# Optimization experiments

Measured on AMD Instinct MI355X. Metric: run time of the kernel, lower is better.

Reference implementation:

```python
import jax, jax.numpy as jnp
import numpy as np

N, E, F, NC, G = 50000, 400000, 128, 10, 64
EPS_BN = 1e-5
NEG_SLOPE = 0.2


def gat_conv(x, src, dst, W, a_src, a_dst, b, H, C):
    # PyG GATConv (concat=True): h = xW reshaped [N,H,C]; edge score =
    # leaky_relu(a_src.h_j + a_dst.h_i); softmax over incoming edges of i;
    # out_i = sum_j alpha_ij * h_j, then bias.
    n = x.shape[0]
    h = (x @ W).reshape(n, H, C)
    s_src = jnp.sum(h * a_src, axis=-1)  # [N,H]
    s_dst = jnp.sum(h * a_dst, axis=-1)  # [N,H]
    e = jax.nn.leaky_relu(s_src[src] + s_dst[dst], NEG_SLOPE)  # [E',H]
    m = jax.ops.segment_max(e, dst, num_segments=n)
    e = jnp.exp(e - m[dst])
    z = jax.ops.segment_sum(e, dst, num_segments=n)
    alpha = e / (z[dst] + 1e-16)
    msg = h[src] * alpha[:, :, None]  # [E',H,C]
    out = jax.ops.segment_sum(msg, dst, num_segments=n)
    return out.reshape(n, H * C) + b


def batch_norm(x, g, b):
    mu = jnp.mean(x, axis=0)
    var = jnp.var(x, axis=0)
    return g * (x - mu) * jax.lax.rsqrt(var + EPS_BN) + b


def setup_inputs() -> dict:
    key = jax.random.key(0)
    ks = jax.random.split(key, 32)
    d = {}
    d["x"] = jax.random.normal(ks[0], (N, F), dtype=jnp.float32)
    d["edge_index"] = jax.random.randint(ks[1], (2, E), 0, N, dtype=jnp.int32)
    d["batch"] = jnp.sort(jax.random.randint(ks[2], (N,), 0, G, dtype=jnp.int32))

    def nrm(k, shape, scale=0.1):
        return jax.random.normal(k, shape, dtype=jnp.float32) * scale

    # GATConv1: F -> 16, heads=20
    d["W1"] = nrm(ks[3], (F, 20 * 16))
    d["as1"] = nrm(ks[4], (20, 16))
    d["ad1"] = nrm(ks[5], (20, 16))
    d["b1"] = jnp.zeros((320,), jnp.float32)
    d["g1"], d["be1"] = jnp.ones((320,), jnp.float32), jnp.zeros((320,), jnp.float32)
    d["lw1"], d["lb1"] = nrm(ks[6], (320, 16)), jnp.zeros((16,), jnp.float32)
    d["gl1"], d["bel1"] = jnp.ones((16,), jnp.float32), jnp.zeros((16,), jnp.float32)
    # GATConv2: 16 -> 32, heads=16
    d["W2"] = nrm(ks[7], (16, 16 * 32))
    d["as2"] = nrm(ks[8], (16, 32))
    d["ad2"] = nrm(ks[9], (16, 32))
    d["b2"] = jnp.zeros((512,), jnp.float32)
    d["g2"], d["be2"] = jnp.ones((512,), jnp.float32), jnp.zeros((512,), jnp.float32)
    d["lw2"], d["lb2"] = nrm(ks[10], (512, 32)), jnp.zeros((32,), jnp.float32)
    d["gl2"], d["bel2"] = jnp.ones((32,), jnp.float32), jnp.zeros((32,), jnp.float32)
    # GATConv3: 32 -> 48, heads=8
    d["W3"] = nrm(ks[11], (32, 8 * 48))
    d["as3"] = nrm(ks[12], (8, 48))
    d["ad3"] = nrm(ks[13], (8, 48))
    d["b3"] = jnp.zeros((384,), jnp.float32)
    d["g3"], d["be3"] = jnp.ones((384,), jnp.float32), jnp.zeros((384,), jnp.float32)
    d["lwf"], d["lbf"] = nrm(ks[14], (384, NC)), jnp.zeros((NC,), jnp.float32)
    return d


def reference(x, edge_index, batch, W1, as1, ad1, b1, g1, be1, lw1, lb1, gl1, bel1,
              W2, as2, ad2, b2, g2, be2, lw2, lb2, gl2, bel2,
              W3, as3, ad3, b3, g3, be3, lwf, lbf):
    n = x.shape[0]
    loops = jnp.arange(n, dtype=edge_index.dtype)
    src = jnp.concatenate([edge_index[0], loops])
    dst = jnp.concatenate([edge_index[1], loops])

    h = gat_conv(x, src, dst, W1, as1, ad1, b1, 20, 16)
    h = jax.nn.relu(batch_norm(h, g1, be1))
    h = h @ lw1 + lb1
    h = jax.nn.relu(batch_norm(h, gl1, bel1))

    h = gat_conv(h, src, dst, W2, as2, ad2, b2, 16, 32)
    h = jax.nn.relu(batch_norm(h, g2, be2))
    h = h @ lw2 + lb2
    h = jax.nn.relu(batch_norm(h, gl2, bel2))

    h = gat_conv(h, src, dst, W3, as3, ad3, b3, 8, 48)
    h = jax.nn.relu(batch_norm(h, g3, be3))

    # global_mean_pool over graph ids
    sums = jax.ops.segment_sum(h, batch, num_segments=G)
    cnts = jax.ops.segment_sum(jnp.ones((n,), h.dtype), batch, num_segments=G)
    pooled = sums / jnp.maximum(cnts, 1.0)[:, None]
    # dropout is identity in eval mode
    return pooled @ lwf + lbf
```

## Files before the change

kernel.cpp:

```cpp
#include <hip/hip_runtime.h>
#include <cstdint>
#include <cstddef>

#define N_NODES 50000
#define N_EDGES 400000
#define TOT_E   450000
#define G_GRAPHS 64
#define PB 2048
#define SCAN_B 98

typedef unsigned short u16;
typedef unsigned int u32;
typedef unsigned char u8;
typedef __attribute__((ext_vector_type(8))) short s16x8;
typedef __attribute__((ext_vector_type(4))) float f32x4;
typedef __attribute__((ext_vector_type(2))) float f32x2;

__device__ __forceinline__ float b2f(u16 v) {
    union { u32 u; float f; } x; x.u = ((u32)v) << 16; return x.f;
}
__device__ __forceinline__ float lo2f(u32 u) {
    union { u32 u; float f; } x; x.u = u << 16; return x.f;
}
__device__ __forceinline__ float hi2f(u32 u) {
    union { u32 u; float f; } x; x.u = u & 0xffff0000u; return x.f;
}
__device__ __forceinline__ u16 f2b(float f) {
    union { float f; u32 u; } x; x.f = f;
    u32 r = x.u + 0x7fffu + ((x.u >> 16) & 1u);
    return (u16)(r >> 16);
}
__device__ __forceinline__ u32 pack2(float a, float b) {
    return (u32)f2b(a) | ((u32)f2b(b) << 16);
}

__global__ void k_init_deg(int* __restrict__ deg) {
    int i = blockIdx.x * blockDim.x + threadIdx.x;
    if (i < N_NODES) deg[i] = 1;
}

__global__ void k_hist(const int* __restrict__ ei, int* __restrict__ deg) {
    int e = blockIdx.x * blockDim.x + threadIdx.x;
    if (e < N_EDGES) atomicAdd(&deg[ei[N_EDGES + e]], 1);
}

__global__ void k_scan1(const int* __restrict__ deg, int* __restrict__ rowptr,
                        int* __restrict__ bsum) {
    __shared__ int buf[512];
    int tid = threadIdx.x;
    int i = blockIdx.x * 512 + tid;
    int v = (i < N_NODES) ? deg[i] : 0;
    buf[tid] = v;
    __syncthreads();
    for (int off = 1; off < 512; off <<= 1) {
        int t = (tid >= off) ? buf[tid - off] : 0;
        __syncthreads();
        buf[tid] += t;
        __syncthreads();
    }
    if (i < N_NODES) rowptr[i] = buf[tid] - v;
    if (tid == 511) bsum[blockIdx.x] = buf[511];
}

__global__ void k_scan2(int* __restrict__ bsum) {
    __shared__ int buf[128];
    int tid = threadIdx.x;
    int v = (tid < SCAN_B) ? bsum[tid] : 0;
    buf[tid] = v;
    __syncthreads();
    for (int off = 1; off < 128; off <<= 1) {
        int t = (tid >= off) ? buf[tid - off] : 0;
        __syncthreads();
        buf[tid] += t;
        __syncthreads();
    }
    if (tid < SCAN_B) bsum[tid] = buf[tid] - v;
}

__global__ void k_scan3(int* __restrict__ rowptr, int* __restrict__ cursor,
                        const int* __restrict__ bsum) {
    int i = blockIdx.x * blockDim.x + threadIdx.x;
    if (i < N_NODES) {
        int v = rowptr[i] + bsum[i >> 9];
        rowptr[i] = v;
        cursor[i] = v;
    }
    if (i == 0) rowptr[N_NODES] = TOT_E;
}

__global__ void k_scatter(const int* __restrict__ ei, int* __restrict__ cursor,
                          int* __restrict__ col, int* __restrict__ cdst) {
    int e = blockIdx.x * blockDim.x + threadIdx.x;
    if (e < N_EDGES) {
        int s = ei[e], d = ei[N_EDGES + e];
        int p = atomicAdd(&cursor[d], 1);
        col[p] = s;
        cdst[p] = d;
    } else if (e < TOT_E) {
        int i = e - N_EDGES;
        int p = atomicAdd(&cursor[i], 1);
        col[p] = i;
        cdst[p] = i;
    }
}

template<int K, int NO>
__global__ void k_wpack(const float* __restrict__ W, u16* __restrict__ Bp) {
    constexpr int KC = (K + 31) / 32;
    constexpr int NT = NO / 16;
    int idx = blockIdx.x * 256 + threadIdx.x;
    if (idx >= KC * NT * 64) return;
    int lane = idx & 63;
    int t = (idx >> 6) % NT;
    int c = (idx >> 6) / NT;
    int n = t * 16 + (lane & 15);
    int kbase = c * 32 + (lane >> 4) * 8;
    u16 v[8];
#pragma unroll
    for (int j = 0; j < 8; j++) {
        int k = kbase + j;
        v[j] = (k < K) ? f2b(W[(size_t)k * NO + n]) : (u16)0;
    }
    *(uint4*)(Bp + (size_t)idx * 8) = *(const uint4*)v;
}

template<int K, int NO, int H, int C>
__global__ void k_wtilde(const float* __restrict__ W, const float* __restrict__ as,
                         const float* __restrict__ ad, float* __restrict__ wts,
                         float* __restrict__ wtd) {
    int t = threadIdx.x;
    if (t >= K * H) return;
    int k = t / H, h = t - k * H;
    float s1 = 0.f, s2 = 0.f;
    for (int c = 0; c < C; c++) {
        float wv = W[(size_t)k * NO + h * C + c];
        s1 = fmaf(wv, as[h * C + c], s1);
        s2 = fmaf(wv, ad[h * C + c], s2);
    }
    wts[h * K + k] = s1;
    wtd[h * K + k] = s2;
}

template<int K>
__global__ void k_xform(const u16* __restrict__ X, const float* __restrict__ sc,
                        const float* __restrict__ sh, u16* __restrict__ Xt) {
    constexpr int NO2 = K / 2;
    int t = blockIdx.x * blockDim.x + threadIdx.x;
    if (t >= N_NODES * NO2) return;
    int w = t % NO2;
    u32 u = ((const u32*)X)[t];
    float2 scv = *(const float2*)&sc[2 * w];
    float2 shv = *(const float2*)&sh[2 * w];
    float a = fmaxf(lo2f(u) * scv.x + shv.x, 0.f);
    float b = fmaxf(hi2f(u) * scv.y + shv.y, 0.f);
    ((u32*)Xt)[t] = pack2(a, b);
}

template<int K, int H>
__global__ void k_scores_x(const u16* __restrict__ Xt, const float* __restrict__ wts,
                           const float* __restrict__ wtd, float* __restrict__ ssrc,
                           float* __restrict__ sdst) {
    int t = blockIdx.x * blockDim.x + threadIdx.x;
    if (t >= N_NODES * H) return;
    int i = t / H, h = t - i * H;
    const uint4* r = (const uint4*)(Xt + (size_t)i * K);
    const float4* ws = (const float4*)(wts + h * K);
    const float4* wd = (const float4*)(wtd + h * K);
    float s1 = 0.f, s2 = 0.f;
#pragma unroll
    for (int c8 = 0; c8 < K / 8; c8++) {
        uint4 u = r[c8];
        float v0 = lo2f(u.x), v1 = hi2f(u.x), v2 = lo2f(u.y), v3 = hi2f(u.y);
        float v4 = lo2f(u.z), v5 = hi2f(u.z), v6 = lo2f(u.w), v7 = hi2f(u.w);
        float4 aa = ws[c8 * 2], ab = ws[c8 * 2 + 1];
        float4 da = wd[c8 * 2], db = wd[c8 * 2 + 1];
        s1 = fmaf(v0, aa.x, fmaf(v1, aa.y, fmaf(v2, aa.z, fmaf(v3, aa.w, s1))));
        s1 = fmaf(v4, ab.x, fmaf(v5, ab.y, fmaf(v6, ab.z, fmaf(v7, ab.w, s1))));
        s2 = fmaf(v0, da.x, fmaf(v1, da.y, fmaf(v2, da.z, fmaf(v3, da.w, s2))));
        s2 = fmaf(v4, db.x, fmaf(v5, db.y, fmaf(v6, db.z, fmaf(v7, db.w, s2))));
    }
    ssrc[t] = s1;
    sdst[t] = s2;
}

template<int H, int K>
__global__ void k_aggx(const u16* __restrict__ Xt, const float* __restrict__ ssrc,
                       const float* __restrict__ sdst, const int* __restrict__ rowptr,
                       const int* __restrict__ col, u16* __restrict__ M) {
    constexpr int WPR = K / 2;
    constexpr int EPR = 64 / WPR;
    constexpr int Q = K / 4;
    static_assert(H * K == 256, "m row must be 256 elems (4/lane)");
    int wid = (int)((blockIdx.x * blockDim.x + threadIdx.x) >> 6);
    int lane = threadIdx.x & 63;
    if (wid >= N_NODES) return;
    int hl = lane / Q;
    int q = lane % Q;
    int lslot = lane / WPR;
    int lword = lane % WPR;
    float sd = (lane < H) ? sdst[(size_t)wid * H + lane] : 0.f;
    float a0 = 0.f, a1 = 0.f, a2 = 0.f, a3 = 0.f;
    float z = 0.f;
    int beg = rowptr[wid], end = rowptr[wid + 1];
    for (int base = beg; base < end; base += 64) {
        int nmax = min(64, end - base);
        int myc = (base + lane < end) ? col[base + lane] : 0;
        int j = 0;
        for (; j + EPR <= nmax; j += EPR) {
            int ce = __shfl(myc, j + lslot);
            u32 g = *(const u32*)(Xt + (size_t)ce * K + lword * 2);
            int se[EPR];
#pragma unroll
            for (int e = 0; e < EPR; e++) se[e] = __shfl(myc, j + e);
            float w[EPR];
#pragma unroll
            for (int e = 0; e < EPR; e++) w[e] = 0.f;
            if (lane < H) {
#pragma unroll
                for (int e = 0; e < EPR; e++) {
                    float v = ssrc[(size_t)se[e] * H + lane] + sd;
                    v = (v > 0.f) ? v : 0.2f * v;
                    w[e] = __expf(v);
                    z += w[e];
                }
            }
#pragma unroll
            for (int e = 0; e < EPR; e++) {
                float al = __shfl(w[e], hl);
                u32 xa = __shfl(g, e * WPR + 2 * q);
                u32 xb = __shfl(g, e * WPR + 2 * q + 1);
                a0 = fmaf(al, lo2f(xa), a0);
                a1 = fmaf(al, hi2f(xa), a1);
                a2 = fmaf(al, lo2f(xb), a2);
                a3 = fmaf(al, hi2f(xb), a3);
            }
        }
        for (; j < nmax; j++) {
            int se = __shfl(myc, j);
            u32 g = *(const u32*)(Xt + (size_t)se * K + lword * 2);
            float w0 = 0.f;
            if (lane < H) {
                float v = ssrc[(size_t)se * H + lane] + sd;
                v = (v > 0.f) ? v : 0.2f * v;
                w0 = __expf(v);
                z += w0;
            }
            float al = __shfl(w0, hl);
            u32 xa = __shfl(g, 2 * q);
            u32 xb = __shfl(g, 2 * q + 1);
            a0 = fmaf(al, lo2f(xa), a0);
            a1 = fmaf(al, hi2f(xa), a1);
            a2 = fmaf(al, lo2f(xb), a2);
            a3 = fmaf(al, hi2f(xb), a3);
        }
    }
    float zk = __shfl(z, hl);
    float inv = 1.0f / (zk + 1e-16f);
    uint2 o;
    o.x = pack2(a0 * inv, a1 * inv);
    o.y = pack2(a2 * inv, a3 * inv);
    u32* orow = (u32*)(M + (size_t)wid * (H * K));
    *(uint2*)&orow[hl * WPR + 2 * q] = o;
}

template<int K, int NO, int C>
__global__ __launch_bounds__(256, 2)
void k_gemmd(const u16* __restrict__ M, const u16* __restrict__ Bp,
             const float* __restrict__ wb, u16* __restrict__ Y) {
    constexpr int NT = NO / 16;
    constexpr int HK = (NO / C) * K;
    int lane = threadIdx.x & 63;
    int wv = __builtin_amdgcn_readfirstlane((int)(threadIdx.x >> 6));
    int rbase = blockIdx.x * 64 + wv * 16;
    int m = lane & 15, quad = lane >> 4;
    int arow = rbase + m;
    if (arow >= N_NODES) arow = N_NODES - 1;
    const u16* xr = M + (size_t)arow * HK;
#pragma unroll
    for (int t = 0; t < NT; t++) {
        int h = (t * 16) / C;
        s16x8 a;
        if (K == 32 || quad < 2) {
            a = *(const s16x8*)(xr + h * K + quad * 8);
        } else {
#pragma unroll
            for (int j = 0; j < 8; j++) a[j] = 0;
        }
        s16x8 b = *(const s16x8*)(Bp + ((size_t)(t * 64 + lane)) * 8);
        f32x4 acc = (f32x4){0.f, 0.f, 0.f, 0.f};
        acc = __builtin_amdgcn_mfma_f32_16x16x32_bf16(a, b, acc, 0, 0, 0);
        int colb = t * 16 + m;
        float bv = wb[colb];
#pragma unroll
        for (int i = 0; i < 4; i++) {
            int grow = rbase + quad * 4 + i;
            if (grow < N_NODES) Y[(size_t)grow * NO + colb] = f2b(acc[i] + bv);
        }
    }
}

template<int K, int NO, bool XFORM>
__global__ __launch_bounds__(256, 2)
void k_gemm(const float* __restrict__ X, const u16* __restrict__ Bp,
            const float* __restrict__ scale, const float* __restrict__ shift,
            u16* __restrict__ Y) {
    constexpr int KC = (K + 31) / 32;
    constexpr int NT = NO / 16;
    int lane = threadIdx.x & 63;
    int wv = __builtin_amdgcn_readfirstlane((int)(threadIdx.x >> 6));
    int rbase = blockIdx.x * 64 + wv * 16;
    int m = lane & 15, quad = lane >> 4;
    int arow = rbase + m;
    if (arow >= N_NODES) arow = N_NODES - 1;
    const float* xr = X + (size_t)arow * K;

    f32x4 acc[NT];
#pragma unroll
    for (int t = 0; t < NT; t++) acc[t] = (f32x4){0.f, 0.f, 0.f, 0.f};

    for (int c = 0; c < KC; c++) {
        int kbase = c * 32 + quad * 8;
        float xv[8];
        if (kbase < K) {
            float4 va = *(const float4*)&xr[kbase];
            float4 vb = *(const float4*)&xr[kbase + 4];
            xv[0] = va.x; xv[1] = va.y; xv[2] = va.z; xv[3] = va.w;
            xv[4] = vb.x; xv[5] = vb.y; xv[6] = vb.z; xv[7] = vb.w;
            if (XFORM) {
                float4 sa = *(const float4*)&scale[kbase];
                float4 sb = *(const float4*)&scale[kbase + 4];
                float4 ha = *(const float4*)&shift[kbase];
                float4 hb = *(const float4*)&shift[kbase + 4];
                xv[0] = fmaxf(xv[0] * sa.x + ha.x, 0.f);
                xv[1] = fmaxf(xv[1] * sa.y + ha.y, 0.f);
                xv[2] = fmaxf(xv[2] * sa.z + ha.z, 0.f);
                xv[3] = fmaxf(xv[3] * sa.w + ha.w, 0.f);
                xv[4] = fmaxf(xv[4] * sb.x + hb.x, 0.f);
                xv[5] = fmaxf(xv[5] * sb.y + hb.y, 0.f);
                xv[6] = fmaxf(xv[6] * sb.z + hb.z, 0.f);
                xv[7] = fmaxf(xv[7] * sb.w + hb.w, 0.f);
            }
        } else {
#pragma unroll
            for (int j = 0; j < 8; j++) xv[j] = 0.f;
        }
        s16x8 a;
#pragma unroll
        for (int j = 0; j < 8; j++) a[j] = (short)f2b(xv[j]);

        const u16* bp = Bp + (size_t)(c * NT) * 64 * 8;
#pragma unroll
        for (int t = 0; t < NT; t++) {
            s16x8 b = *(const s16x8*)(bp + ((size_t)(t * 64 + lane)) * 8);
            acc[t] = __builtin_amdgcn_mfma_f32_16x16x32_bf16(a, b, acc[t], 0, 0, 0);
        }
    }

#pragma unroll
    for (int t = 0; t < NT; t++) {
        int colb = t * 16 + m;
#pragma unroll
        for (int i = 0; i < 4; i++) {
            int grow = rbase + quad * 4 + i;
            if (grow < N_NODES) Y[(size_t)grow * NO + colb] = f2b(acc[t][i]);
        }
    }
}

template<int K, int NO, bool XFORM, bool BIAS>
__global__ __launch_bounds__(256, 2)
void k_gemmb(const u16* __restrict__ X, const u16* __restrict__ Bp,
             const float* __restrict__ scale, const float* __restrict__ shift,
             const float* __restrict__ wb, u16* __restrict__ Y) {
    constexpr int KC = (K + 31) / 32;
    constexpr int NT = NO / 16;
    int lane = threadIdx.x & 63;
    int wv = __builtin_amdgcn_readfirstlane((int)(threadIdx.x >> 6));
    int rbase = blockIdx.x * 64 + wv * 16;
    int m = lane & 15, quad = lane >> 4;
    int arow = rbase + m;
    if (arow >= N_NODES) arow = N_NODES - 1;
    const u32* xr = (const u32*)(X + (size_t)arow * K);

    f32x4 acc[NT];
#pragma unroll
    for (int t = 0; t < NT; t++) acc[t] = (f32x4){0.f, 0.f, 0.f, 0.f};

    for (int c = 0; c < KC; c++) {
        int kbase = c * 32 + quad * 8;
        s16x8 a;
        if (kbase < K) {
            uint4 w = *(const uint4*)&xr[kbase >> 1];
            if (XFORM) {
                float xv[8];
                xv[0] = lo2f(w.x); xv[1] = hi2f(w.x);
                xv[2] = lo2f(w.y); xv[3] = hi2f(w.y);
                xv[4] = lo2f(w.z); xv[5] = hi2f(w.z);
                xv[6] = lo2f(w.w); xv[7] = hi2f(w.w);
                float4 sa = *(const float4*)&scale[kbase];
                float4 sb = *(const float4*)&scale[kbase + 4];
                float4 ha = *(const float4*)&shift[kbase];
                float4 hb = *(const float4*)&shift[kbase + 4];
                xv[0] = fmaxf(xv[0] * sa.x + ha.x, 0.f);
                xv[1] = fmaxf(xv[1] * sa.y + ha.y, 0.f);
                xv[2] = fmaxf(xv[2] * sa.z + ha.z, 0.f);
                xv[3] = fmaxf(xv[3] * sa.w + ha.w, 0.f);
                xv[4] = fmaxf(xv[4] * sb.x + hb.x, 0.f);
                xv[5] = fmaxf(xv[5] * sb.y + hb.y, 0.f);
                xv[6] = fmaxf(xv[6] * sb.z + hb.z, 0.f);
                xv[7] = fmaxf(xv[7] * sb.w + hb.w, 0.f);
#pragma unroll
                for (int j = 0; j < 8; j++) a[j] = (short)f2b(xv[j]);
            } else {
                a = *(const s16x8*)&w;
            }
        } else {
#pragma unroll
            for (int j = 0; j < 8; j++) a[j] = 0;
        }

        const u16* bp = Bp + (size_t)(c * NT) * 64 * 8;
#pragma unroll
        for (int t = 0; t < NT; t++) {
            s16x8 b = *(const s16x8*)(bp + ((size_t)(t * 64 + lane)) * 8);
            acc[t] = __builtin_amdgcn_mfma_f32_16x16x32_bf16(a, b, acc[t], 0, 0, 0);
        }
    }

#pragma unroll
    for (int t = 0; t < NT; t++) {
        int colb = t * 16 + m;
        float bv = BIAS ? wb[colb] : 0.f;
#pragma unroll
        for (int i = 0; i < 4; i++) {
            int grow = rbase + quad * 4 + i;
            if (grow < N_NODES) Y[(size_t)grow * NO + colb] = f2b(acc[t][i] + bv);
        }
    }
}

template<int H, int C>
__global__ void k_scores(const u16* __restrict__ Hm, const float* __restrict__ asrc,
                         const float* __restrict__ adst, float* __restrict__ ssrc,
                         float* __restrict__ sdst, u8* __restrict__ H8) {
    static_assert(C == 16, "fp8 emit assumes C==16");
    int t = blockIdx.x * blockDim.x + threadIdx.x;
    if (t >= N_NODES * H) return;
    int i = t / H, h = t - i * H;
    const uint4* row4 = (const uint4*)(Hm + (size_t)i * H * C + h * C);
    const float4* a4 = (const float4*)(asrc + h * C);
    const float4* d4 = (const float4*)(adst + h * C);
    float s1 = 0.f, s2 = 0.f;
    uint4 q8;
    u32* qw = (u32*)&q8;
#pragma unroll
    for (int c8 = 0; c8 < C / 8; c8++) {
        uint4 u = row4[c8];
        float v0 = lo2f(u.x), v1 = hi2f(u.x), v2 = lo2f(u.y), v3 = hi2f(u.y);
        float v4 = lo2f(u.z), v5 = hi2f(u.z), v6 = lo2f(u.w), v7 = hi2f(u.w);
        float4 aa = a4[c8 * 2], ab = a4[c8 * 2 + 1];
        float4 da = d4[c8 * 2], db = d4[c8 * 2 + 1];
        s1 = fmaf(v0, aa.x, fmaf(v1, aa.y, fmaf(v2, aa.z, fmaf(v3, aa.w, s1))));
        s1 = fmaf(v4, ab.x, fmaf(v5, ab.y, fmaf(v6, ab.z, fmaf(v7, ab.w, s1))));
        s2 = fmaf(v0, da.x, fmaf(v1, da.y, fmaf(v2, da.z, fmaf(v3, da.w, s2))));
        s2 = fmaf(v4, db.x, fmaf(v5, db.y, fmaf(v6, db.z, fmaf(v7, db.w, s2))));
        u32 qa = 0, qb = 0;
        qa = __builtin_amdgcn_cvt_pk_fp8_f32(v0, v1, qa, false);
        qa = __builtin_amdgcn_cvt_pk_fp8_f32(v2, v3, qa, true);
        qb = __builtin_amdgcn_cvt_pk_fp8_f32(v4, v5, qb, false);
        qb = __builtin_amdgcn_cvt_pk_fp8_f32(v6, v7, qb, true);
        qw[c8 * 2] = qa;
        qw[c8 * 2 + 1] = qb;
    }
    ssrc[t] = s1;
    sdst[t] = s2;
    *(uint4*)(H8 + (size_t)i * (H * C) + h * C) = q8;
}

template<int H, int C>
__global__ void k_agg8(const u8* __restrict__ Hm8, const float* __restrict__ ssrc,
                       const float* __restrict__ sdst, const int* __restrict__ rowptr,
                       const int* __restrict__ col, const float* __restrict__ bias,
                       u16* __restrict__ out) {
    constexpr int HC = H * C;
    constexpr int W2 = HC / 8;
    static_assert(W2 <= 64, "row must fit 64 uint2");
    static_assert((C % 8) == 0, "8-col block must stay within one head");
    int wid = (int)((blockIdx.x * blockDim.x + threadIdx.x) >> 6);
    int lane = threadIdx.x & 63;
    if (wid >= N_NODES) return;
    int hl = (8 * lane) / C;
    int gidx = (lane < W2) ? lane : 0;
    float sd = (lane < H) ? sdst[(size_t)wid * H + lane] : 0.f;
    float acc[8];
#pragma unroll
    for (int q = 0; q < 8; q++) acc[q] = 0.f;
    float z = 0.f;
    int beg = rowptr[wid], end = rowptr[wid + 1];
    for (int base = beg; base < end; base += 64) {
        int nmax = min(64, end - base);
        int myc = (base + lane < end) ? col[base + lane] : 0;
        int j = 0;
        for (; j + 4 <= nmax; j += 4) {
            int s0 = __shfl(myc, j), s1 = __shfl(myc, j + 1);
            int s2 = __shfl(myc, j + 2), s3 = __shfl(myc, j + 3);
            uint2 g0 = ((const uint2*)(Hm8 + (size_t)s0 * HC))[gidx];
            uint2 g1 = ((const uint2*)(Hm8 + (size_t)s1 * HC))[gidx];
            uint2 g2 = ((const uint2*)(Hm8 + (size_t)s2 * HC))[gidx];
            uint2 g3 = ((const uint2*)(Hm8 + (size_t)s3 * HC))[gidx];
            float w0 = 0.f, w1 = 0.f, w2 = 0.f, w3 = 0.f;
            if (lane < H) {
                float v0 = ssrc[(size_t)s0 * H + lane] + sd;
                float v1 = ssrc[(size_t)s1 * H + lane] + sd;
                float v2 = ssrc[(size_t)s2 * H + lane] + sd;
                float v3 = ssrc[(size_t)s3 * H + lane] + sd;
                v0 = (v0 > 0.f) ? v0 : 0.2f * v0;
                v1 = (v1 > 0.f) ? v1 : 0.2f * v1;
                v2 = (v2 > 0.f) ? v2 : 0.2f * v2;
                v3 = (v3 > 0.f) ? v3 : 0.2f * v3;
                w0 = __expf(v0); w1 = __expf(v1);
                w2 = __expf(v2); w3 = __expf(v3);
                z += (w0 + w1) + (w2 + w3);
            }
            float wk0 = __shfl(w0, hl), wk1 = __shfl(w1, hl);
            float wk2 = __shfl(w2, hl), wk3 = __shfl(w3, hl);
            f32x2 p;
            p = __builtin_amdgcn_cvt_pk_f32_fp8(g0.x, false);
            acc[0] = fmaf(wk0, p.x, acc[0]); acc[1] = fmaf(wk0, p.y, acc[1]);
            p = __builtin_amdgcn_cvt_pk_f32_fp8(g0.x, true);
            acc[2] = fmaf(wk0, p.x, acc[2]); acc[3] = fmaf(wk0, p.y, acc[3]);
            p = __builtin_amdgcn_cvt_pk_f32_fp8(g0.y, false);
            acc[4] = fmaf(wk0, p.x, acc[4]); acc[5] = fmaf(wk0, p.y, acc[5]);
            p = __builtin_amdgcn_cvt_pk_f32_fp8(g0.y, true);
            acc[6] = fmaf(wk0, p.x, acc[6]); acc[7] = fmaf(wk0, p.y, acc[7]);
            p = __builtin_amdgcn_cvt_pk_f32_fp8(g1.x, false);
            acc[0] = fmaf(wk1, p.x, acc[0]); acc[1] = fmaf(wk1, p.y, acc[1]);
            p = __builtin_amdgcn_cvt_pk_f32_fp8(g1.x, true);
            acc[2] = fmaf(wk1, p.x, acc[2]); acc[3] = fmaf(wk1, p.y, acc[3]);
            p = __builtin_amdgcn_cvt_pk_f32_fp8(g1.y, false);
            acc[4] = fmaf(wk1, p.x, acc[4]); acc[5] = fmaf(wk1, p.y, acc[5]);
            p = __builtin_amdgcn_cvt_pk_f32_fp8(g1.y, true);
            acc[6] = fmaf(wk1, p.x, acc[6]); acc[7] = fmaf(wk1, p.y, acc[7]);
            p = __builtin_amdgcn_cvt_pk_f32_fp8(g2.x, false);
            acc[0] = fmaf(wk2, p.x, acc[0]); acc[1] = fmaf(wk2, p.y, acc[1]);
            p = __builtin_amdgcn_cvt_pk_f32_fp8(g2.x, true);
            acc[2] = fmaf(wk2, p.x, acc[2]); acc[3] = fmaf(wk2, p.y, acc[3]);
            p = __builtin_amdgcn_cvt_pk_f32_fp8(g2.y, false);
            acc[4] = fmaf(wk2, p.x, acc[4]); acc[5] = fmaf(wk2, p.y, acc[5]);
            p = __builtin_amdgcn_cvt_pk_f32_fp8(g2.y, true);
            acc[6] = fmaf(wk2, p.x, acc[6]); acc[7] = fmaf(wk2, p.y, acc[7]);
            p = __builtin_amdgcn_cvt_pk_f32_fp8(g3.x, false);
            acc[0] = fmaf(wk3, p.x, acc[0]); acc[1] = fmaf(wk3, p.y, acc[1]);
            p = __builtin_amdgcn_cvt_pk_f32_fp8(g3.x, true);
            acc[2] = fmaf(wk3, p.x, acc[2]); acc[3] = fmaf(wk3, p.y, acc[3]);
            p = __builtin_amdgcn_cvt_pk_f32_fp8(g3.y, false);
            acc[4] = fmaf(wk3, p.x, acc[4]); acc[5] = fmaf(wk3, p.y, acc[5]);
            p = __builtin_amdgcn_cvt_pk_f32_fp8(g3.y, true);
            acc[6] = fmaf(wk3, p.x, acc[6]); acc[7] = fmaf(wk3, p.y, acc[7]);
        }
        for (; j < nmax; j++) {
            int s0 = __shfl(myc, j);
            uint2 g0 = ((const uint2*)(Hm8 + (size_t)s0 * HC))[gidx];
            float w0 = 0.f;
            if (lane < H) {
                float v = ssrc[(size_t)s0 * H + lane] + sd;
                v = (v > 0.f) ? v : 0.2f * v;
                w0 = __expf(v);
                z += w0;
            }
            float wk0 = __shfl(w0, hl);
            f32x2 p;
            p = __builtin_amdgcn_cvt_pk_f32_fp8(g0.x, false);
            acc[0] = fmaf(wk0, p.x, acc[0]); acc[1] = fmaf(wk0, p.y, acc[1]);
            p = __builtin_amdgcn_cvt_pk_f32_fp8(g0.x, true);
            acc[2] = fmaf(wk0, p.x, acc[2]); acc[3] = fmaf(wk0, p.y, acc[3]);
            p = __builtin_amdgcn_cvt_pk_f32_fp8(g0.y, false);
            acc[4] = fmaf(wk0, p.x, acc[4]); acc[5] = fmaf(wk0, p.y, acc[5]);
            p = __builtin_amdgcn_cvt_pk_f32_fp8(g0.y, true);
            acc[6] = fmaf(wk0, p.x, acc[6]); acc[7] = fmaf(wk0, p.y, acc[7]);
        }
    }
    float zk = __shfl(z, hl);
    if (lane < W2) {
        float inv = 1.0f / (zk + 1e-16f);
        const float4* b4 = (const float4*)(bias + 8 * lane);
        float4 ba = b4[0], bb = b4[1];
        uint4 o;
        o.x = pack2(fmaf(acc[0], inv, ba.x), fmaf(acc[1], inv, ba.y));
        o.y = pack2(fmaf(acc[2], inv, ba.z), fmaf(acc[3], inv, ba.w));
        o.z = pack2(fmaf(acc[4], inv, bb.x), fmaf(acc[5], inv, bb.y));
        o.w = pack2(fmaf(acc[6], inv, bb.z), fmaf(acc[7], inv, bb.w));
        ((uint4*)(out + (size_t)wid * HC))[lane] = o;
    }
}

template<int NO>
__global__ void k_bnstats(const u16* __restrict__ X, float* __restrict__ psum,
                          float* __restrict__ psumsq) {
    constexpr int NO2 = NO / 2;
    constexpr int RPS = (NO2 >= 256) ? 1 : ((255 + NO2) / NO2);
    constexpr int BS = NO2 * RPS;
    __shared__ float2 ls[BS], ls2[BS];
    int c2 = threadIdx.x % NO2;
    int rsub = threadIdx.x / NO2;
    constexpr int chunk = (N_NODES + PB - 1) / PB;
    int r0 = blockIdx.x * chunk;
    int r1 = min(N_NODES, r0 + chunk);
    float2 s = make_float2(0.f, 0.f), s2 = make_float2(0.f, 0.f);
    const u32* Xw = (const u32*)X;
#pragma unroll 4
    for (int r = r0 + rsub; r < r1; r += RPS) {
        u32 u = Xw[(size_t)r * NO2 + c2];
        float a = lo2f(u), b = hi2f(u);
        s.x += a; s.y += b;
        s2.x += a * a; s2.y += b * b;
    }
    if (RPS > 1) {
        ls[threadIdx.x] = s;
        ls2[threadIdx.x] = s2;
        __syncthreads();
        for (int off = BS / 2; off >= NO2; off >>= 1) {
            if (threadIdx.x < off) {
                ls[threadIdx.x].x += ls[threadIdx.x + off].x;
                ls[threadIdx.x].y += ls[threadIdx.x + off].y;
                ls2[threadIdx.x].x += ls2[threadIdx.x + off].x;
                ls2[threadIdx.x].y += ls2[threadIdx.x + off].y;
            }
            __syncthreads();
        }
        s = ls[threadIdx.x];
        s2 = ls2[threadIdx.x];
    }
    if (rsub == 0) {
        *(float2*)&psum[(size_t)blockIdx.x * NO + 2 * c2] = s;
        *(float2*)&psumsq[(size_t)blockIdx.x * NO + 2 * c2] = s2;
    }
}

__global__ void k_bnfinal(const float* __restrict__ psum, const float* __restrict__ psumsq,
                          const float* __restrict__ g, const float* __restrict__ be,
                          float* __restrict__ scale, float* __restrict__ shift, int NO) {
    __shared__ float s1[256], s2[256];
    int col = blockIdx.x;
    int tid = threadIdx.x;
    float a = 0.f, b = 0.f;
    for (int bk = tid; bk < PB; bk += 256) {
        a += psum[(size_t)bk * NO + col];
        b += psumsq[(size_t)bk * NO + col];
    }
    s1[tid] = a;
    s2[tid] = b;
    __syncthreads();
    for (int off = 128; off > 0; off >>= 1) {
        if (tid < off) {
            s1[tid] += s1[tid + off];
            s2[tid] += s2[tid + off];
        }
        __syncthreads();
    }
    if (tid == 0) {
        float mu = s1[0] / (float)N_NODES;
        float var = s2[0] / (float)N_NODES - mu * mu;
        float sc = g[col] * rsqrtf(var + 1e-5f);
        scale[col] = sc;
        shift[col] = be[col] - mu * sc;
    }
}

__global__ void k_bhist(const int* __restrict__ batch, int* __restrict__ cnt) {
    __shared__ int h[G_GRAPHS];
    int tid = threadIdx.x;
    if (tid < G_GRAPHS) h[tid] = 0;
    __syncthreads();
    int i = blockIdx.x * blockDim.x + tid;
    if (i < N_NODES) atomicAdd(&h[batch[i]], 1);
    __syncthreads();
    if (tid < G_GRAPHS) atomicAdd(&cnt[tid], h[tid]);
}

__global__ void k_pool(const u16* __restrict__ X, const int* __restrict__ batch,
                       const float* __restrict__ sc, const float* __restrict__ sh,
                       float* __restrict__ pooled) {
    int t2 = threadIdx.x;
    const int chunk = (N_NODES + gridDim.x - 1) / gridDim.x;
    int r0 = blockIdx.x * chunk;
    int r1 = min(N_NODES, r0 + chunk);
    if (r0 >= N_NODES) return;
    float2 scv = *(const float2*)&sc[2 * t2];
    float2 shv = *(const float2*)&sh[2 * t2];
    const u32* Xw = (const u32*)X;
    float2 acc = make_float2(0.f, 0.f);
    int cur = batch[r0];
    for (int r = r0; r < r1; r++) {
        int gid = batch[r];
        if (gid != cur) {
            atomicAdd(&pooled[(size_t)cur * 384 + 2 * t2], acc.x);
            atomicAdd(&pooled[(size_t)cur * 384 + 2 * t2 + 1], acc.y);
            acc = make_float2(0.f, 0.f);
            cur = gid;
        }
        u32 u = Xw[(size_t)r * 192 + t2];
        acc.x += fmaxf(lo2f(u) * scv.x + shv.x, 0.f);
        acc.y += fmaxf(hi2f(u) * scv.y + shv.y, 0.f);
    }
    atomicAdd(&pooled[(size_t)cur * 384 + 2 * t2], acc.x);
    atomicAdd(&pooled[(size_t)cur * 384 + 2 * t2 + 1], acc.y);
}

__global__ void k_final(const float* __restrict__ pooled, const int* __restrict__ cnt,
                        const float* __restrict__ lwf, const float* __restrict__ lbf,
                        float* __restrict__ out) {
    int t = threadIdx.x;
    if (t >= G_GRAPHS * 10) return;
    int g = t / 10, c = t - g * 10;
    float inv = 1.0f / fmaxf((float)cnt[g], 1.0f);
    float acc = lbf[c];
    for (int k = 0; k < 384; k++)
        acc = fmaf(pooled[(size_t)g * 384 + k] * inv, lwf[k * 10 + c], acc);
    out[t] = acc;
}

extern "C" void kernel_launch(void* const* d_in, const int* in_sizes, int n_in,
                              void* d_out, int out_size, void* d_ws, size_t ws_size,
                              hipStream_t stream) {
    const float* x    = (const float*)d_in[0];
    const int*   ei   = (const int*)d_in[1];
    const int*   batch= (const int*)d_in[2];
    const float* W1   = (const float*)d_in[3];
    const float* as1  = (const float*)d_in[4];
    const float* ad1  = (const float*)d_in[5];
    const float* b1   = (const float*)d_in[6];
    const float* g1   = (const float*)d_in[7];
    const float* be1  = (const float*)d_in[8];
    const float* lw1  = (const float*)d_in[9];
    const float* lb1  = (const float*)d_in[10];
    const float* gl1  = (const float*)d_in[11];
    const float* bel1 = (const float*)d_in[12];
    const float* W2   = (const float*)d_in[13];
    const float* as2  = (const float*)d_in[14];
    const float* ad2  = (const float*)d_in[15];
    const float* b2   = (const float*)d_in[16];
    const float* g2   = (const float*)d_in[17];
    const float* be2  = (const float*)d_in[18];
    const float* lw2  = (const float*)d_in[19];
    const float* lb2  = (const float*)d_in[20];
    const float* gl2  = (const float*)d_in[21];
    const float* bel2 = (const float*)d_in[22];
    const float* W3   = (const float*)d_in[23];
    const float* as3  = (const float*)d_in[24];
    const float* ad3  = (const float*)d_in[25];
    const float* b3   = (const float*)d_in[26];
    const float* g3   = (const float*)d_in[27];
    const float* be3  = (const float*)d_in[28];
    const float* lwf  = (const float*)d_in[29];
    const float* lbf  = (const float*)d_in[30];
    float* out = (float*)d_out;

    char* p = (char*)d_ws;
    auto alloc = [&](size_t bytes) {
        char* r = p;
        p += (bytes + 255) & ~(size_t)255;
        return r;
    };
    int*   rowptr = (int*)alloc(4 * (size_t)(N_NODES + 1));
    int*   cursor = (int*)alloc(4 * (size_t)N_NODES);
    int*   deg    = (int*)alloc(4 * (size_t)N_NODES);
    int*   bsum   = (int*)alloc(4 * (size_t)(SCAN_B + 1));
    int*   col    = (int*)alloc(4 * (size_t)TOT_E);
    int*   cdst   = (int*)alloc(4 * (size_t)TOT_E);
    float* ssrc   = (float*)alloc(4 * (size_t)N_NODES * 20);
    float* sdst   = (float*)alloc(4 * (size_t)N_NODES * 20);
    u16*   hbuf   = (u16*)alloc(2 * (size_t)N_NODES * 512);
    u16*   obuf   = (u16*)alloc(2 * (size_t)N_NODES * 512);
    u16*   xbuf   = (u16*)alloc(2 * (size_t)N_NODES * 32);
    u16*   xtil   = (u16*)alloc(2 * (size_t)N_NODES * 32);
    u8*    hbuf8  = (u8*)alloc((size_t)N_NODES * 320);
    float* psum   = (float*)alloc(4 * (size_t)PB * 512);
    float* psumsq = (float*)alloc(4 * (size_t)PB * 512);
    float* scA    = (float*)alloc(4 * 512);
    float* shA    = (float*)alloc(4 * 512);
    float* scB    = (float*)alloc(4 * 64);
    float* shB    = (float*)alloc(4 * 64);
    float* wts    = (float*)alloc(4 * 256);
    float* wtd    = (float*)alloc(4 * 256);
    float* pooled = (float*)alloc(4 * (size_t)G_GRAPHS * 384);
    int*   cnt    = (int*)alloc(4 * G_GRAPHS);
    u16*   bp1    = (u16*)alloc(2 * (size_t)4 * 20 * 64 * 8);
    u16*   bp2    = (u16*)alloc(2 * (size_t)1 * 32 * 64 * 8);
    u16*   bp3    = (u16*)alloc(2 * (size_t)1 * 24 * 64 * 8);
    u16*   bpl1   = (u16*)alloc(2 * (size_t)10 * 1 * 64 * 8);
    u16*   bpl2   = (u16*)alloc(2 * (size_t)16 * 2 * 64 * 8);
    u16*   mbuf   = hbuf;

    const int LB = (N_NODES + 63) / 64;

    k_init_deg<<<(N_NODES + 255) / 256, 256, 0, stream>>>(deg);
    k_hist<<<(N_EDGES + 255) / 256, 256, 0, stream>>>(ei, deg);
    k_scan1<<<SCAN_B, 512, 0, stream>>>(deg, rowptr, bsum);
    k_scan2<<<1, 128, 0, stream>>>(bsum);
    k_scan3<<<(N_NODES + 255) / 256, 256, 0, stream>>>(rowptr, cursor, bsum);
    k_scatter<<<(TOT_E + 255) / 256, 256, 0, stream>>>(ei, cursor, col, cdst);
    k_wpack<128, 320><<<20, 256, 0, stream>>>(W1, bp1);
    k_wpack<16, 512><<<8, 256, 0, stream>>>(W2, bp2);
    k_wpack<32, 384><<<6, 256, 0, stream>>>(W3, bp3);
    k_wpack<320, 16><<<3, 256, 0, stream>>>(lw1, bpl1);
    k_wpack<512, 32><<<8, 256, 0, stream>>>(lw2, bpl2);
    hipMemsetAsync(pooled, 0, 4 * (size_t)G_GRAPHS * 384 + 256, stream);

    k_gemm<128, 320, false><<<LB, 256, 0, stream>>>(x, bp1, nullptr, nullptr, hbuf);
    k_scores<20, 16><<<(N_NODES * 20 + 255) / 256, 256, 0, stream>>>(hbuf, as1, ad1, ssrc, sdst, hbuf8);
    k_agg8<20, 16><<<(N_NODES + 3) / 4, 256, 0, stream>>>(hbuf8, ssrc, sdst, rowptr, col, b1, obuf);
    k_bnstats<320><<<PB, 320, 0, stream>>>(obuf, psum, psumsq);
    k_bnfinal<<<320, 256, 0, stream>>>(psum, psumsq, g1, be1, scA, shA, 320);
    k_gemmb<320, 16, true, true><<<LB, 256, 0, stream>>>(obuf, bpl1, scA, shA, lb1, xbuf);
    k_bnstats<16><<<PB, 256, 0, stream>>>(xbuf, psum, psumsq);
    k_bnfinal<<<16, 256, 0, stream>>>(psum, psumsq, gl1, bel1, scB, shB, 16);

    k_wtilde<16, 512, 16, 32><<<1, 256, 0, stream>>>(W2, as2, ad2, wts, wtd);
    k_xform<16><<<(N_NODES * 8 + 255) / 256, 256, 0, stream>>>(xbuf, scB, shB, xtil);
    k_scores_x<16, 16><<<(N_NODES * 16 + 255) / 256, 256, 0, stream>>>(xtil, wts, wtd, ssrc, sdst);
    k_aggx<16, 16><<<(N_NODES + 3) / 4, 256, 0, stream>>>(xtil, ssrc, sdst, rowptr, col, mbuf);
    k_gemmd<16, 512, 32><<<LB, 256, 0, stream>>>(mbuf, bp2, b2, obuf);
    k_bnstats<512><<<PB, 256, 0, stream>>>(obuf, psum, psumsq);
    k_bnfinal<<<512, 256, 0, stream>>>(psum, psumsq, g2, be2, scA, shA, 512);
    k_gemmb<512, 32, true, true><<<LB, 256, 0, stream>>>(obuf, bpl2, scA, shA, lb2, xbuf);
    k_bnstats<32><<<PB, 256, 0, stream>>>(xbuf, psum, psumsq);
    k_bnfinal<<<32, 256, 0, stream>>>(psum, psumsq, gl2, bel2, scB, shB, 32);

    k_wtilde<32, 384, 8, 48><<<1, 256, 0, stream>>>(W3, as3, ad3, wts, wtd);
    k_xform<32><<<(N_NODES * 16 + 255) / 256, 256, 0, stream>>>(xbuf, scB, shB, xtil);
    k_scores_x<32, 8><<<(N_NODES * 8 + 255) / 256, 256, 0, stream>>>(xtil, wts, wtd, ssrc, sdst);
    k_aggx<8, 32><<<(N_NODES + 3) / 4, 256, 0, stream>>>(xtil, ssrc, sdst, rowptr, col, mbuf);
    k_gemmd<32, 384, 48><<<LB, 256, 0, stream>>>(mbuf, bp3, b3, obuf);
    k_bnstats<384><<<PB, 384, 0, stream>>>(obuf, psum, psumsq);
    k_bnfinal<<<384, 256, 0, stream>>>(psum, psumsq, g3, be3, scA, shA, 384);

    k_bhist<<<(N_NODES + 255) / 256, 256, 0, stream>>>(batch, cnt);
    k_pool<<<2048, 192, 0, stream>>>(obuf, batch, scA, shA, pooled);
    k_final<<<1, 640, 0, stream>>>(pooled, cnt, lwf, lbf, out);
}
```

Baseline: 584.7 us.

## Fuse BN statistics into GAT output GEMM epilogue and vectorize aggregation FMAs

The layer-2 and layer-3 output GEMMs now accumulate per-column sum and sum-of-squares in shared memory and atomically add them to a global buffer. This removes the separate bnstats pass over the 50000x512 and 50000x384 outputs and replaces the multi-block bnfinal with a single-block finalizer. The aggregation kernels switch their accumulators to packed float2 vectors to encourage packed FMA instructions. The final linear layer spreads each output over a wavefront with a shuffle reduction, and k_wtilde uses split accumulators. Risks: float atomics make the statistics order-dependent, and E[x^2]-mu^2 variance is less numerically stable.

```diff
diff --git a/kernel.cpp b/kernel.cpp
--- a/kernel.cpp
+++ b/kernel.cpp
@@ -128,17 +128,24 @@
 __global__ void k_wtilde(const float* __restrict__ W, const float* __restrict__ as,
                          const float* __restrict__ ad, float* __restrict__ wts,
                          float* __restrict__ wtd) {
+    static_assert((C % 4) == 0, "C divisible by 4");
     int t = threadIdx.x;
     if (t >= K * H) return;
     int k = t / H, h = t - k * H;
-    float s1 = 0.f, s2 = 0.f;
-    for (int c = 0; c < C; c++) {
-        float wv = W[(size_t)k * NO + h * C + c];
-        s1 = fmaf(wv, as[h * C + c], s1);
-        s2 = fmaf(wv, ad[h * C + c], s2);
-    }
-    wts[h * K + k] = s1;
-    wtd[h * K + k] = s2;
+    float s1a = 0.f, s1b = 0.f, s1c = 0.f, s1d = 0.f;
+    float s2a = 0.f, s2b = 0.f, s2c = 0.f, s2d = 0.f;
+    const float* wr = W + (size_t)k * NO + h * C;
+    const float* ar = as + h * C;
+    const float* dr = ad + h * C;
+    for (int c = 0; c < C; c += 4) {
+        float w0 = wr[c], w1 = wr[c + 1], w2 = wr[c + 2], w3 = wr[c + 3];
+        s1a = fmaf(w0, ar[c], s1a);     s1b = fmaf(w1, ar[c + 1], s1b);
+        s1c = fmaf(w2, ar[c + 2], s1c); s1d = fmaf(w3, ar[c + 3], s1d);
+        s2a = fmaf(w0, dr[c], s2a);     s2b = fmaf(w1, dr[c + 1], s2b);
+        s2c = fmaf(w2, dr[c + 2], s2c); s2d = fmaf(w3, dr[c + 3], s2d);
+    }
+    wts[h * K + k] = (s1a + s1b) + (s1c + s1d);
+    wtd[h * K + k] = (s2a + s2b) + (s2c + s2d);
 }
 
 template<int K>
@@ -199,7 +206,7 @@
     int lslot = lane / WPR;
     int lword = lane % WPR;
     float sd = (lane < H) ? sdst[(size_t)wid * H + lane] : 0.f;
-    float a0 = 0.f, a1 = 0.f, a2 = 0.f, a3 = 0.f;
+    f32x2 acc01 = {0.f, 0.f}, acc23 = {0.f, 0.f};
     float z = 0.f;
     int beg = rowptr[wid], end = rowptr[wid + 1];
     for (int base = beg; base < end; base += 64) {
@@ -229,10 +236,11 @@
                 float al = __shfl(w[e], hl);
                 u32 xa = __shfl(g, e * WPR + 2 * q);
                 u32 xb = __shfl(g, e * WPR + 2 * q + 1);
-                a0 = fmaf(al, lo2f(xa), a0);
-                a1 = fmaf(al, hi2f(xa), a1);
-                a2 = fmaf(al, lo2f(xb), a2);
-                a3 = fmaf(al, hi2f(xb), a3);
+                f32x2 al2 = {al, al};
+                f32x2 xa2 = {lo2f(xa), hi2f(xa)};
+                f32x2 xb2 = {lo2f(xb), hi2f(xb)};
+                acc01 += xa2 * al2;
+                acc23 += xb2 * al2;
             }
         }
         for (; j < nmax; j++) {
@@ -248,17 +256,18 @@
             float al = __shfl(w0, hl);
             u32 xa = __shfl(g, 2 * q);
             u32 xb = __shfl(g, 2 * q + 1);
-            a0 = fmaf(al, lo2f(xa), a0);
-            a1 = fmaf(al, hi2f(xa), a1);
-            a2 = fmaf(al, lo2f(xb), a2);
-            a3 = fmaf(al, hi2f(xb), a3);
+            f32x2 al2 = {al, al};
+            f32x2 xa2 = {lo2f(xa), hi2f(xa)};
+            f32x2 xb2 = {lo2f(xb), hi2f(xb)};
+            acc01 += xa2 * al2;
+            acc23 += xb2 * al2;
         }
     }
     float zk = __shfl(z, hl);
     float inv = 1.0f / (zk + 1e-16f);
     uint2 o;
-    o.x = pack2(a0 * inv, a1 * inv);
-    o.y = pack2(a2 * inv, a3 * inv);
+    o.x = pack2(acc01.x * inv, acc01.y * inv);
+    o.y = pack2(acc23.x * inv, acc23.y * inv);
     u32* orow = (u32*)(M + (size_t)wid * (H * K));
     *(uint2*)&orow[hl * WPR + 2 * q] = o;
 }
@@ -266,9 +275,14 @@
 template<int K, int NO, int C>
 __global__ __launch_bounds__(256, 2)
 void k_gemmd(const u16* __restrict__ M, const u16* __restrict__ Bp,
-             const float* __restrict__ wb, u16* __restrict__ Y) {
+             const float* __restrict__ wb, u16* __restrict__ Y,
+             float* __restrict__ pst) {
     constexpr int NT = NO / 16;
     constexpr int HK = (NO / C) * K;
+    __shared__ float ls[2 * NO];
+    int tid = threadIdx.x;
+    for (int i = tid; i < 2 * NO; i += 256) ls[i] = 0.f;
+    __syncthreads();
     int lane = threadIdx.x & 63;
     int wv = __builtin_amdgcn_readfirstlane((int)(threadIdx.x >> 6));
     int rbase = blockIdx.x * 64 + wv * 16;
@@ -291,12 +305,38 @@
         acc = __builtin_amdgcn_mfma_f32_16x16x32_bf16(a, b, acc, 0, 0, 0);
         int colb = t * 16 + m;
         float bv = wb[colb];
+        float s = 0.f, q = 0.f;
 #pragma unroll
         for (int i = 0; i < 4; i++) {
             int grow = rbase + quad * 4 + i;
-            if (grow < N_NODES) Y[(size_t)grow * NO + colb] = f2b(acc[i] + bv);
-        }
-    }
+            float v = acc[i] + bv;
+            if (grow < N_NODES) {
+                Y[(size_t)grow * NO + colb] = f2b(v);
+                s += v;
+                q += v * v;
+            }
+        }
+        s += __shfl_xor(s, 16); s += __shfl_xor(s, 32);
+        q += __shfl_xor(q, 16); q += __shfl_xor(q, 32);
+        if (quad == 0) {
+            atomicAdd(&ls[colb], s);
+            atomicAdd(&ls[NO + colb], q);
+        }
+    }
+    __syncthreads();
+    for (int i = tid; i < 2 * NO; i += 256) atomicAdd(&pst[i], ls[i]);
+}
+
+__global__ void k_bnfinal2(const float* __restrict__ pst, const float* __restrict__ g,
+                           const float* __restrict__ be, float* __restrict__ scale,
+                           float* __restrict__ shift, int NO) {
+    int t = threadIdx.x;
+    if (t >= NO) return;
+    float mu = pst[t] / (float)N_NODES;
+    float var = pst[NO + t] / (float)N_NODES - mu * mu;
+    float sc = g[t] * rsqrtf(var + 1e-5f);
+    scale[t] = sc;
+    shift[t] = be[t] - mu * sc;
 }
 
 template<int K, int NO, bool XFORM>
@@ -492,11 +532,16 @@
     int hl = (8 * lane) / C;
     int gidx = (lane < W2) ? lane : 0;
     float sd = (lane < H) ? sdst[(size_t)wid * H + lane] : 0.f;
-    float acc[8];
-#pragma unroll
-    for (int q = 0; q < 8; q++) acc[q] = 0.f;
+    f32x2 acc01 = {0.f, 0.f}, acc23 = {0.f, 0.f};
+    f32x2 acc45 = {0.f, 0.f}, acc67 = {0.f, 0.f};
     float z = 0.f;
     int beg = rowptr[wid], end = rowptr[wid + 1];
+#define ACC8(gg, wk) { \
+        f32x2 wv_ = {wk, wk}; \
+        acc01 += __builtin_amdgcn_cvt_pk_f32_fp8(gg.x, false) * wv_; \
+        acc23 += __builtin_amdgcn_cvt_pk_f32_fp8(gg.x, true) * wv_; \
+        acc45 += __builtin_amdgcn_cvt_pk_f32_fp8(gg.y, false) * wv_; \
+        acc67 += __builtin_amdgcn_cvt_pk_f32_fp8(gg.y, true) * wv_; }
     for (int base = beg; base < end; base += 64) {
         int nmax = min(64, end - base);
         int myc = (base + lane < end) ? col[base + lane] : 0;
@@ -524,39 +569,10 @@
             }
             float wk0 = __shfl(w0, hl), wk1 = __shfl(w1, hl);
             float wk2 = __shfl(w2, hl), wk3 = __shfl(w3, hl);
-            f32x2 p;
-            p = __builtin_amdgcn_cvt_pk_f32_fp8(g0.x, false);
-            acc[0] = fmaf(wk0, p.x, acc[0]); acc[1] = fmaf(wk0, p.y, acc[1]);
-            p = __builtin_amdgcn_cvt_pk_f32_fp8(g0.x, true);
-            acc[2] = fmaf(wk0, p.x, acc[2]); acc[3] = fmaf(wk0, p.y, acc[3]);
-            p = __builtin_amdgcn_cvt_pk_f32_fp8(g0.y, false);
-            acc[4] = fmaf(wk0, p.x, acc[4]); acc[5] = fmaf(wk0, p.y, acc[5]);
-            p = __builtin_amdgcn_cvt_pk_f32_fp8(g0.y, true);
-            acc[6] = fmaf(wk0, p.x, acc[6]); acc[7] = fmaf(wk0, p.y, acc[7]);
-            p = __builtin_amdgcn_cvt_pk_f32_fp8(g1.x, false);
-            acc[0] = fmaf(wk1, p.x, acc[0]); acc[1] = fmaf(wk1, p.y, acc[1]);
-            p = __builtin_amdgcn_cvt_pk_f32_fp8(g1.x, true);
-            acc[2] = fmaf(wk1, p.x, acc[2]); acc[3] = fmaf(wk1, p.y, acc[3]);
-            p = __builtin_amdgcn_cvt_pk_f32_fp8(g1.y, false);
-            acc[4] = fmaf(wk1, p.x, acc[4]); acc[5] = fmaf(wk1, p.y, acc[5]);
-            p = __builtin_amdgcn_cvt_pk_f32_fp8(g1.y, true);
-            acc[6] = fmaf(wk1, p.x, acc[6]); acc[7] = fmaf(wk1, p.y, acc[7]);
-            p = __builtin_amdgcn_cvt_pk_f32_fp8(g2.x, false);
-            acc[0] = fmaf(wk2, p.x, acc[0]); acc[1] = fmaf(wk2, p.y, acc[1]);
-            p = __builtin_amdgcn_cvt_pk_f32_fp8(g2.x, true);
-            acc[2] = fmaf(wk2, p.x, acc[2]); acc[3] = fmaf(wk2, p.y, acc[3]);
-            p = __builtin_amdgcn_cvt_pk_f32_fp8(g2.y, false);
-            acc[4] = fmaf(wk2, p.x, acc[4]); acc[5] = fmaf(wk2, p.y, acc[5]);
-            p = __builtin_amdgcn_cvt_pk_f32_fp8(g2.y, true);
-            acc[6] = fmaf(wk2, p.x, acc[6]); acc[7] = fmaf(wk2, p.y, acc[7]);
-            p = __builtin_amdgcn_cvt_pk_f32_fp8(g3.x, false);
-            acc[0] = fmaf(wk3, p.x, acc[0]); acc[1] = fmaf(wk3, p.y, acc[1]);
-            p = __builtin_amdgcn_cvt_pk_f32_fp8(g3.x, true);
-            acc[2] = fmaf(wk3, p.x, acc[2]); acc[3] = fmaf(wk3, p.y, acc[3]);
-            p = __builtin_amdgcn_cvt_pk_f32_fp8(g3.y, false);
-            acc[4] = fmaf(wk3, p.x, acc[4]); acc[5] = fmaf(wk3, p.y, acc[5]);
-            p = __builtin_amdgcn_cvt_pk_f32_fp8(g3.y, true);
-            acc[6] = fmaf(wk3, p.x, acc[6]); acc[7] = fmaf(wk3, p.y, acc[7]);
+            ACC8(g0, wk0)
+            ACC8(g1, wk1)
+            ACC8(g2, wk2)
+            ACC8(g3, wk3)
         }
         for (; j < nmax; j++) {
             int s0 = __shfl(myc, j);
@@ -569,27 +585,20 @@
                 z += w0;
             }
             float wk0 = __shfl(w0, hl);
-            f32x2 p;
-            p = __builtin_amdgcn_cvt_pk_f32_fp8(g0.x, false);
-            acc[0] = fmaf(wk0, p.x, acc[0]); acc[1] = fmaf(wk0, p.y, acc[1]);
-            p = __builtin_amdgcn_cvt_pk_f32_fp8(g0.x, true);
-            acc[2] = fmaf(wk0, p.x, acc[2]); acc[3] = fmaf(wk0, p.y, acc[3]);
-            p = __builtin_amdgcn_cvt_pk_f32_fp8(g0.y, false);
-            acc[4] = fmaf(wk0, p.x, acc[4]); acc[5] = fmaf(wk0, p.y, acc[5]);
-            p = __builtin_amdgcn_cvt_pk_f32_fp8(g0.y, true);
-            acc[6] = fmaf(wk0, p.x, acc[6]); acc[7] = fmaf(wk0, p.y, acc[7]);
-        }
-    }
+            ACC8(g0, wk0)
+        }
+    }
+#undef ACC8
     float zk = __shfl(z, hl);
     if (lane < W2) {
         float inv = 1.0f / (zk + 1e-16f);
         const float4* b4 = (const float4*)(bias + 8 * lane);
         float4 ba = b4[0], bb = b4[1];
         uint4 o;
-        o.x = pack2(fmaf(acc[0], inv, ba.x), fmaf(acc[1], inv, ba.y));
-        o.y = pack2(fmaf(acc[2], inv, ba.z), fmaf(acc[3], inv, ba.w));
-        o.z = pack2(fmaf(acc[4], inv, bb.x), fmaf(acc[5], inv, bb.y));
-        o.w = pack2(fmaf(acc[6], inv, bb.z), fmaf(acc[7], inv, bb.w));
+        o.x = pack2(fmaf(acc01.x, inv, ba.x), fmaf(acc01.y, inv, ba.y));
+        o.y = pack2(fmaf(acc23.x, inv, ba.z), fmaf(acc23.y, inv, ba.w));
+        o.z = pack2(fmaf(acc45.x, inv, bb.x), fmaf(acc45.y, inv, bb.y));
+        o.w = pack2(fmaf(acc67.x, inv, bb.z), fmaf(acc67.y, inv, bb.w));
         ((uint4*)(out + (size_t)wid * HC))[lane] = o;
     }
 }
@@ -710,14 +719,17 @@
 __global__ void k_final(const float* __restrict__ pooled, const int* __restrict__ cnt,
                         const float* __restrict__ lwf, const float* __restrict__ lbf,
                         float* __restrict__ out) {
-    int t = threadIdx.x;
-    if (t >= G_GRAPHS * 10) return;
-    int g = t / 10, c = t - g * 10;
+    int wid = (int)((blockIdx.x * blockDim.x + threadIdx.x) >> 6);
+    int lane = threadIdx.x & 63;
+    if (wid >= G_GRAPHS * 10) return;
+    int g = wid / 10, c = wid - g * 10;
     float inv = 1.0f / fmaxf((float)cnt[g], 1.0f);
-    float acc = lbf[c];
-    for (int k = 0; k < 384; k++)
-        acc = fmaf(pooled[(size_t)g * 384 + k] * inv, lwf[k * 10 + c], acc);
-    out[t] = acc;
+    float acc = 0.f;
+    for (int k = lane; k < 384; k += 64)
+        acc += pooled[(size_t)g * 384 + k] * lwf[k * 10 + c];
+#pragma unroll
+    for (int off = 32; off > 0; off >>= 1) acc += __shfl_xor(acc, off);
+    if (lane == 0) out[wid] = acc * inv + lbf[c];
 }
 
 extern "C" void kernel_launch(void* const* d_in, const int* in_sizes, int n_in,
@@ -783,6 +795,9 @@
     float* shB    = (float*)alloc(4 * 64);
     float* wts    = (float*)alloc(4 * 256);
     float* wtd    = (float*)alloc(4 * 256);
+    float* pstat  = (float*)alloc(4 * 1792);
+    float* pst512 = pstat;
+    float* pst384 = pstat + 1024;
     float* pooled = (float*)alloc(4 * (size_t)G_GRAPHS * 384);
     int*   cnt    = (int*)alloc(4 * G_GRAPHS);
     u16*   bp1    = (u16*)alloc(2 * (size_t)4 * 20 * 64 * 8);
@@ -806,6 +821,7 @@
     k_wpack<320, 16><<<3, 256, 0, stream>>>(lw1, bpl1);
     k_wpack<512, 32><<<8, 256, 0, stream>>>(lw2, bpl2);
     hipMemsetAsync(pooled, 0, 4 * (size_t)G_GRAPHS * 384 + 256, stream);
+    hipMemsetAsync(pstat, 0, 4 * 1792, stream);
 
     k_gemm<128, 320, false><<<LB, 256, 0, stream>>>(x, bp1, nullptr, nullptr, hbuf);
     k_scores<20, 16><<<(N_NODES * 20 + 255) / 256, 256, 0, stream>>>(hbuf, as1, ad1, ssrc, sdst, hbuf8);
@@ -820,9 +836,8 @@
     k_xform<16><<<(N_NODES * 8 + 255) / 256, 256, 0, stream>>>(xbuf, scB, shB, xtil);
     k_scores_x<16, 16><<<(N_NODES * 16 + 255) / 256, 256, 0, stream>>>(xtil, wts, wtd, ssrc, sdst);
     k_aggx<16, 16><<<(N_NODES + 3) / 4, 256, 0, stream>>>(xtil, ssrc, sdst, rowptr, col, mbuf);
-    k_gemmd<16, 512, 32><<<LB, 256, 0, stream>>>(mbuf, bp2, b2, obuf);
-    k_bnstats<512><<<PB, 256, 0, stream>>>(obuf, psum, psumsq);
-    k_bnfinal<<<512, 256, 0, stream>>>(psum, psumsq, g2, be2, scA, shA, 512);
+    k_gemmd<16, 512, 32><<<LB, 256, 0, stream>>>(mbuf, bp2, b2, obuf, pst512);
+    k_bnfinal2<<<1, 512, 0, stream>>>(pst512, g2, be2, scA, shA, 512);
     k_gemmb<512, 32, true, true><<<LB, 256, 0, stream>>>(obuf, bpl2, scA, shA, lb2, xbuf);
     k_bnstats<32><<<PB, 256, 0, stream>>>(xbuf, psum, psumsq);
     k_bnfinal<<<32, 256, 0, stream>>>(psum, psumsq, gl2, bel2, scB, shB, 32);
@@ -831,11 +846,10 @@
     k_xform<32><<<(N_NODES * 16 + 255) / 256, 256, 0, stream>>>(xbuf, scB, shB, xtil);
     k_scores_x<32, 8><<<(N_NODES * 8 + 255) / 256, 256, 0, stream>>>(xtil, wts, wtd, ssrc, sdst);
     k_aggx<8, 32><<<(N_NODES + 3) / 4, 256, 0, stream>>>(xtil, ssrc, sdst, rowptr, col, mbuf);
-    k_gemmd<32, 384, 48><<<LB, 256, 0, stream>>>(mbuf, bp3, b3, obuf);
-    k_bnstats<384><<<PB, 384, 0, stream>>>(obuf, psum, psumsq);
-    k_bnfinal<<<384, 256, 0, stream>>>(psum, psumsq, g3, be3, scA, shA, 384);
+    k_gemmd<32, 384, 48><<<LB, 256, 0, stream>>>(mbuf, bp3, b3, obuf, pst384);
+    k_bnfinal2<<<1, 512, 0, stream>>>(pst384, g3, be3, scA, shA, 384);
 
     k_bhist<<<(N_NODES + 255) / 256, 256, 0, stream>>>(batch, cnt);
     k_pool<<<2048, 192, 0, stream>>>(obuf, batch, scA, shA, pooled);
-    k_final<<<1, 640, 0, stream>>>(pooled, cnt, lwf, lbf, out);
-}
+    k_final<<<160, 256, 0, stream>>>(pooled, cnt, lwf, lbf, out);
+}
```

Measured after the change: 558.7 us. 1.05x faster.
